# Optimization experiments

Measured on AMD Instinct MI355X. Metric: run time of the kernel, lower is better.

The kernel has to match this reference:

```python
import jax, jax.numpy as jnp
import numpy as np

B, S, D, H, HD = 2, 2048, 1024, 16, 64
K, L = 1024, 4  # num_codes, vq_levels


def setup_inputs() -> dict:
    key = jax.random.key(0)
    ks = jax.random.split(key, 12)
    w = lambda k, shape: jax.random.normal(k, shape, jnp.float32) * 0.02
    return {
        "x": jax.random.normal(ks[0], (B, S, D), jnp.float32),
        "ln1_g": jnp.ones((D,), jnp.float32), "ln1_b": jnp.zeros((D,), jnp.float32),
        "wq": w(ks[1], (D, D)), "wk": w(ks[2], (D, D)), "wv": w(ks[3], (D, D)),
        "wg": w(ks[4], (D, D)), "wo": w(ks[5], (D, D)),
        "ln2_g": jnp.ones((D,), jnp.float32), "ln2_b": jnp.zeros((D,), jnp.float32),
        "w1": w(ks[6], (D, 4 * D)), "b1": jnp.zeros((4 * D,), jnp.float32),
        "w2": w(ks[7], (4 * D, D)), "b2": jnp.zeros((D,), jnp.float32),
        "ln3_g": jnp.ones((D,), jnp.float32), "ln3_b": jnp.zeros((D,), jnp.float32),
        "codebooks": jax.random.uniform(ks[8], (L, K, D), jnp.float32, -1.0 / K, 1.0 / K),
    }


def _ln(x, g, b):
    m = jnp.mean(x, -1, keepdims=True)
    v = jnp.var(x, -1, keepdims=True)
    return (x - m) / jnp.sqrt(v + 1e-5) * g + b


def _rope(x):  # x: [B, S, H, HD]
    hd = x.shape[-1]
    inv = 1.0 / (10000.0 ** (jnp.arange(0, hd, 2, dtype=jnp.float32) / hd))
    t = jnp.arange(x.shape[1], dtype=jnp.float32)
    f = jnp.einsum('i,j->ij', t, inv)               # [S, HD/2]
    emb = jnp.concatenate([f, f], -1)               # [S, HD]
    cos = jnp.cos(emb)[None, :, None, :]
    sin = jnp.sin(emb)[None, :, None, :]
    x1, x2 = jnp.split(x, 2, -1)
    rot = jnp.concatenate([-x2, x1], -1)
    return x * cos + rot * sin


def reference(x, ln1_g, ln1_b, wq, wk, wv, wg, wo, ln2_g, ln2_b,
              w1, b1, w2, b2, ln3_g, ln3_b, codebooks):
    # --- retention sub-block (pre-LN) ---
    h = _ln(x, ln1_g, ln1_b)
    q = (h @ wq).reshape(B, S, H, HD)
    k = (h @ wk).reshape(B, S, H, HD)
    v = (h @ wv).reshape(B, S, H, HD)
    q, k = _rope(q), _rope(k)
    q, k, v = (a.transpose(0, 2, 1, 3) for a in (q, k, v))  # [B,H,S,HD]
    i = jnp.arange(S)
    dmask = jnp.tril(i[:, None] - i[None, :]).astype(jnp.float32)  # [S,S], >=0
    gamma = (1.0 - jnp.exp2(-5.0 - jnp.arange(H, dtype=jnp.float32)))[:, None, None]
    decay = (gamma ** dmask) * jnp.tril(jnp.ones((S, S), jnp.float32))  # [H,S,S]
    ret = jnp.einsum('bhqd,bhkd->bhqk', q, k) / np.sqrt(HD).astype(np.float32) * decay
    o = jnp.einsum('bhqk,bhkd->bhqd', ret, v).transpose(0, 2, 1, 3).reshape(B, S, D)
    g = jax.nn.silu(h @ wg)
    x = x + (o * g) @ wo
    # --- MLP sub-block (pre-LN) ---
    h2 = _ln(x, ln2_g, ln2_b)
    x = x + (jax.nn.gelu(h2 @ w1 + b1, approximate=False) @ w2 + b2)
    # --- residual vector quantizer ---
    xn = _ln(x, ln3_g, ln3_b)
    residual, total = xn, jnp.zeros_like(xn)
    ql, el = 0.0, 0.0
    for lvl in range(L):
        cb = codebooks[lvl]                         # [K, D]
        flat = residual.reshape(-1, D)              # [B*S, D]
        d2 = (jnp.sum(flat ** 2, 1, keepdims=True)
              + jnp.sum(cb ** 2, 1) - 2.0 * flat @ cb.T)
        idx = jnp.argmin(d2, 1)
        quant = cb[idx].reshape(xn.shape)
        ql = ql + jnp.mean((quant - jax.lax.stop_gradient(residual)) ** 2)
        el = el + jnp.mean((jax.lax.stop_gradient(quant) - residual) ** 2)
        total = total + quant
        residual = residual - jax.lax.stop_gradient(quant)
    final = xn + jax.lax.stop_gradient(total - xn)  # straight-through
    return (x + final, ql / L, el / L)
```

## Files before the change

### kernel.cpp

```cpp
#include <hip/hip_runtime.h>
#include <cstdint>
#include <cstddef>

#define DEV __device__ __forceinline__

typedef __attribute__((ext_vector_type(8))) short bf16x8;
typedef __attribute__((ext_vector_type(4))) float f32x4;

typedef const __attribute__((address_space(1))) void gl_void;
typedef __attribute__((address_space(3))) void lds_void;

DEV unsigned short f2bf(float f){
  union { float f; uint32_t u; } v; v.f = f;
  uint32_t r = v.u + 0x7FFFu + ((v.u >> 16) & 1u);
  return (unsigned short)(r >> 16);
}
DEV float bf2f(unsigned short u){
  union { uint32_t u; float f; } v; v.u = ((uint32_t)u) << 16; return v.f;
}
DEV uint32_t packbf2(float a, float b){
  return (uint32_t)f2bf(a) | ((uint32_t)f2bf(b) << 16);
}

__global__ void ln_kernel(const float* __restrict__ x, const float* __restrict__ gw,
                          const float* __restrict__ bw, unsigned short* __restrict__ obf,
                          float* __restrict__ of32)
{
  const int row = blockIdx.x, t = threadIdx.x;
  const float4 v = ((const float4*)(x + (size_t)row*1024))[t];
  float s  = v.x + v.y + v.z + v.w;
  float s2 = v.x*v.x + v.y*v.y + v.z*v.z + v.w*v.w;
  #pragma unroll
  for (int o = 32; o >= 1; o >>= 1){ s += __shfl_down(s, o); s2 += __shfl_down(s2, o); }
  __shared__ float red[8];
  const int w = t >> 6, ln = t & 63;
  if (ln == 0){ red[w] = s; red[4+w] = s2; }
  __syncthreads();
  const float fs  = red[0]+red[1]+red[2]+red[3];
  const float fs2 = red[4]+red[5]+red[6]+red[7];
  const float mean = fs * (1.0f/1024.0f);
  const float var  = fs2 * (1.0f/1024.0f) - mean*mean;
  const float rstd = rsqrtf(var + 1e-5f);
  const float4 gv = ((const float4*)gw)[t];
  const float4 bv = ((const float4*)bw)[t];
  float4 o4;
  o4.x = (v.x-mean)*rstd*gv.x + bv.x;
  o4.y = (v.y-mean)*rstd*gv.y + bv.y;
  o4.z = (v.z-mean)*rstd*gv.z + bv.z;
  o4.w = (v.w-mean)*rstd*gv.w + bv.w;
  if (of32) ((float4*)(of32 + (size_t)row*1024))[t] = o4;
  ushort4 ob; ob.x = f2bf(o4.x); ob.y = f2bf(o4.y); ob.z = f2bf(o4.z); ob.w = f2bf(o4.w);
  ((ushort4*)(obf + (size_t)row*1024))[t] = ob;
}

__global__ void reduce_ln(const float* __restrict__ p, const float* __restrict__ b2,
                          const float* __restrict__ x1, float* __restrict__ x2,
                          const float* __restrict__ g3, const float* __restrict__ b3,
                          unsigned short* __restrict__ resb, float* __restrict__ xnf)
{
  const int row = blockIdx.x, t = threadIdx.x;
  const size_t off = (size_t)row*1024/4 + t;
  const float4 a = ((const float4*)p)[off];
  const float4 b = ((const float4*)(p + 4194304))[off];
  const float4 rv = ((const float4*)x1)[off];
  const float4 bv2 = ((const float4*)b2)[t];
  float4 v;
  v.x = a.x + b.x + rv.x + bv2.x;
  v.y = a.y + b.y + rv.y + bv2.y;
  v.z = a.z + b.z + rv.z + bv2.z;
  v.w = a.w + b.w + rv.w + bv2.w;
  ((float4*)x2)[off] = v;
  float s  = v.x + v.y + v.z + v.w;
  float s2 = v.x*v.x + v.y*v.y + v.z*v.z + v.w*v.w;
  #pragma unroll
  for (int o = 32; o >= 1; o >>= 1){ s += __shfl_down(s, o); s2 += __shfl_down(s2, o); }
  __shared__ float red[8];
  const int w = t >> 6, ln = t & 63;
  if (ln == 0){ red[w] = s; red[4+w] = s2; }
  __syncthreads();
  const float fs  = red[0]+red[1]+red[2]+red[3];
  const float fs2 = red[4]+red[5]+red[6]+red[7];
  const float mean = fs * (1.0f/1024.0f);
  const float var  = fs2 * (1.0f/1024.0f) - mean*mean;
  const float rstd = rsqrtf(var + 1e-5f);
  const float4 gv = ((const float4*)g3)[t];
  const float4 bv = ((const float4*)b3)[t];
  float4 o4;
  o4.x = (v.x-mean)*rstd*gv.x + bv.x;
  o4.y = (v.y-mean)*rstd*gv.y + bv.y;
  o4.z = (v.z-mean)*rstd*gv.z + bv.z;
  o4.w = (v.w-mean)*rstd*gv.w + bv.w;
  ((float4*)xnf)[off] = o4;
  ushort4 ob; ob.x = f2bf(o4.x); ob.y = f2bf(o4.y); ob.z = f2bf(o4.z); ob.w = f2bf(o4.w);
  ((ushort4*)resb)[off] = ob;
}

struct Ptr5 { const float* p[5]; };

DEV void dev_transpose(const float* __restrict__ src, unsigned short* __restrict__ dst,
                       int r0, int c0, int R, int C)
{
  __shared__ float tile[32][33];
  const int tx = threadIdx.x & 31, ty = threadIdx.x >> 5;
  #pragma unroll
  for (int i = 0; i < 32; i += 8)
    tile[ty+i][tx] = src[(size_t)(r0+ty+i)*C + c0 + tx];
  __syncthreads();
  #pragma unroll
  for (int i = 0; i < 32; i += 8)
    dst[(size_t)(c0+ty+i)*R + r0 + tx] = f2bf(tile[tx][ty+i]);
}

__global__ void prep_all(Ptr5 p5, unsigned short* __restrict__ wqkvgT,
                         const float* __restrict__ w1, unsigned short* __restrict__ w1T,
                         const float* __restrict__ w2, unsigned short* __restrict__ w2T,
                         const float* __restrict__ cb, unsigned short* __restrict__ cbbf,
                         float* __restrict__ cbn2, float2* __restrict__ rtab,
                         const float* __restrict__ x, const float* __restrict__ ln1_g,
                         const float* __restrict__ ln1_b, unsigned short* __restrict__ hbf)
{
  const int b = blockIdx.x, t = threadIdx.x;
  if (b < 5120){
    const int z = b >> 10, r = b & 1023;
    dev_transpose(p5.p[z], wqkvgT + (size_t)z*1048576, (r >> 5)*32, (r & 31)*32, 1024, 1024);
  } else if (b < 9216){
    const int r = b - 5120;
    dev_transpose(w1, w1T, (r >> 7)*32, (r & 127)*32, 1024, 4096);
  } else if (b < 13312){
    const int r = b - 9216;
    dev_transpose(w2, w2T, (r >> 5)*32, (r & 31)*32, 4096, 1024);
  } else if (b < 17408){
    const int code = b - 13312;
    const float4 v = ((const float4*)(cb + (size_t)code*1024))[t];
    ushort4 o; o.x = f2bf(v.x); o.y = f2bf(v.y); o.z = f2bf(v.z); o.w = f2bf(v.w);
    ((ushort4*)(cbbf + (size_t)code*1024))[t] = o;
    float s = v.x*v.x + v.y*v.y + v.z*v.z + v.w*v.w;
    #pragma unroll
    for (int off = 32; off >= 1; off >>= 1) s += __shfl_down(s, off);
    __shared__ float red[4];
    if ((t & 63) == 0) red[t >> 6] = s;
    __syncthreads();
    if (t == 0) cbn2[code] = red[0]+red[1]+red[2]+red[3];
  } else if (b < 17664){
    const int i = (b - 17408)*256 + t;
    const int s = i >> 5, j = i & 31;
    const float ang = (float)s * exp2f(-(float)j * 0.4152410118609203f);
    float sn, cs; sincosf(ang, &sn, &cs);
    rtab[i] = make_float2(cs, sn);
  } else {
    const int row = b - 17664;
    const float4 v = ((const float4*)(x + (size_t)row*1024))[t];
    float s  = v.x + v.y + v.z + v.w;
    float s2 = v.x*v.x + v.y*v.y + v.z*v.z + v.w*v.w;
    #pragma unroll
    for (int o = 32; o >= 1; o >>= 1){ s += __shfl_down(s, o); s2 += __shfl_down(s2, o); }
    __shared__ float red2[8];
    const int w = t >> 6, ln = t & 63;
    if (ln == 0){ red2[w] = s; red2[4+w] = s2; }
    __syncthreads();
    const float fs  = red2[0]+red2[1]+red2[2]+red2[3];
    const float fs2 = red2[4]+red2[5]+red2[6]+red2[7];
    const float mean = fs * (1.0f/1024.0f);
    const float var  = fs2 * (1.0f/1024.0f) - mean*mean;
    const float rstd = rsqrtf(var + 1e-5f);
    const float4 gv = ((const float4*)ln1_g)[t];
    const float4 bv = ((const float4*)ln1_b)[t];
    ushort4 ob;
    ob.x = f2bf((v.x-mean)*rstd*gv.x + bv.x);
    ob.y = f2bf((v.y-mean)*rstd*gv.y + bv.y);
    ob.z = f2bf((v.z-mean)*rstd*gv.z + bv.z);
    ob.w = f2bf((v.w-mean)*rstd*gv.w + bv.w);
    ((ushort4*)(hbf + (size_t)row*1024))[t] = ob;
  }
}

template<int EPI>
__global__ __launch_bounds__(512, 2) void gemm256(
    const unsigned short* __restrict__ A, const unsigned short* __restrict__ BT,
    unsigned short* __restrict__ C, const float* __restrict__ bias,
    const float2* __restrict__ rt, int M, int N, int K)
{
  __shared__ __align__(16) unsigned short SH[65536];
  const int t = threadIdx.x;
  const int w = t >> 6, ln = t & 63, lg = ln >> 4, lc = ln & 15;
  const int wm = w >> 2, wn = w & 3;
  const int gx = gridDim.x, nwg = gridDim.x * gridDim.y;
  int lin = blockIdx.y * gx + blockIdx.x;
  lin = (lin >> 3) + (lin & 7) * (nwg >> 3);
  const int m0 = (lin / gx) * 256, n0 = (lin % gx) * 256;
  const int NT = K >> 6;
  const int nit = NT >> 1;

  f32x4 acc[2][2][4][2] = {};
  bf16x8 aF[4][2], bF[2][2];

  auto stageHT = [&](int d, int isB, int h, int kt){
    const unsigned short* src = isB ? BT : A;
    const int mb = (isB ? n0 : m0) + h*128;
    const int base16 = isB*4096 + d*2048 + h*1024;
    #pragma unroll
    for (int j = 0; j < 2; ++j){
      const int o = j*512 + t;
      const int wu = o & 63;
      const int r16 = wu >> 2, cu = wu & 3;
      const int s = o >> 6;
      const int rg = s >> 1, cg = s & 1;
      const int row = rg*16 + r16;
      const int srcu = cg*4 + (cu ^ ((r16 & 8) >> 2));
      __builtin_amdgcn_global_load_lds(
        (gl_void*)(src + (size_t)(mb + row)*K + (size_t)kt*64 + srcu*8),
        (lds_void*)&SH[(base16 + j*512 + (t & ~63))*8], 16, 0, 0);
    }
  };

  auto ldA = [&](int d, int mh, int mf, int ks) -> bf16x8 {
    const int u = d*2048 + mh*1024 + ((wm*4+mf)*2 + ks)*64 + lc*4 + (lg ^ ((lc & 8) >> 2));
    return *(const bf16x8*)&SH[u*8];
  };
  auto ldB = [&](int d, int nh, int nf, int ks) -> bf16x8 {
    const int u = 4096 + d*2048 + nh*1024 + ((wn*2+nf)*2 + ks)*64 + lc*4 + (lg ^ ((lc & 8) >> 2));
    return *(const bf16x8*)&SH[u*8];
  };

#define RD_A(d, mh) { _Pragma("unroll") for (int mf = 0; mf < 4; ++mf){ \
    aF[mf][0] = ldA(d, mh, mf, 0); aF[mf][1] = ldA(d, mh, mf, 1); } }
#define RD_B(d, nh) { _Pragma("unroll") for (int nf = 0; nf < 2; ++nf){ \
    bF[nf][0] = ldB(d, nh, nf, 0); bF[nf][1] = ldB(d, nh, nf, 1); } }
#define MM(mh, nh) { \
    __builtin_amdgcn_s_setprio(1); \
    _Pragma("unroll") for (int mf = 0; mf < 4; ++mf) \
      _Pragma("unroll") for (int nf = 0; nf < 2; ++nf){ \
        acc[mh][nh][mf][nf] = __builtin_amdgcn_mfma_f32_16x16x32_bf16(aF[mf][0], bF[nf][0], acc[mh][nh][mf][nf], 0, 0, 0); \
        acc[mh][nh][mf][nf] = __builtin_amdgcn_mfma_f32_16x16x32_bf16(aF[mf][1], bF[nf][1], acc[mh][nh][mf][nf], 0, 0, 0); } \
    __builtin_amdgcn_s_setprio(0); }
#define BAR()   __builtin_amdgcn_s_barrier()
#define LGKM0() asm volatile("s_waitcnt lgkmcnt(0)" ::: "memory")

  stageHT(0,0,0,0); stageHT(0,0,1,0); stageHT(0,1,0,0); stageHT(0,1,1,0);
  stageHT(1,0,0,1); stageHT(1,1,1,1);
  asm volatile("s_waitcnt vmcnt(4)" ::: "memory");
  BAR();

  for (int it = 0; it < nit; ++it){
    const int v = 2*it + 1, up = 2*it + 2, vp = 2*it + 3;
    const bool hu = (up < NT), hv = (vp < NT);

    RD_A(0,0); RD_B(0,0);
    stageHT(1,0,1,v);
    BAR(); LGKM0(); MM(0,0); BAR();

    RD_B(0,1);
    stageHT(1,1,0,v);
    BAR(); LGKM0(); MM(0,1); BAR();

    RD_A(0,1);
    if (hu) stageHT(0,0,0,up);
    BAR(); LGKM0(); MM(1,1); BAR();

    RD_B(0,0);
    if (hu) stageHT(0,1,1,up);
    BAR(); LGKM0(); MM(1,0);
    if (hu) asm volatile("s_waitcnt vmcnt(4)" ::: "memory");
    else    asm volatile("s_waitcnt vmcnt(0)" ::: "memory");
    BAR();

    RD_A(1,0); RD_B(1,0);
    if (hu) stageHT(0,0,1,up);
    BAR(); LGKM0(); MM(0,0); BAR();

    RD_B(1,1);
    if (hu) stageHT(0,1,0,up);
    BAR(); LGKM0(); MM(0,1); BAR();

    RD_A(1,1);
    if (hv) stageHT(1,0,0,vp);
    BAR(); LGKM0(); MM(1,1); BAR();

    RD_B(1,0);
    if (hv) stageHT(1,1,1,vp);
    BAR(); LGKM0(); MM(1,0);
    if (hv) asm volatile("s_waitcnt vmcnt(4)" ::: "memory");
    else    asm volatile("s_waitcnt vmcnt(0)" ::: "memory");
    BAR();
  }
#undef RD_A
#undef RD_B
#undef MM

  const int sect = n0 >> 10;
  unsigned short* outp3 = C + (size_t)sect*4194304;
  const int cb1 = n0 & 1023;
  unsigned short* slab = &SH[wm*4096];

  #pragma unroll
  for (int mh = 0; mh < 2; ++mh){
    #pragma unroll
    for (int mf = 0; mf < 4; ++mf){
      BAR();
      #pragma unroll
      for (int nh = 0; nh < 2; ++nh)
        #pragma unroll
        for (int nf = 0; nf < 2; ++nf)
          #pragma unroll
          for (int r = 0; r < 4; ++r){
            const int rho = lg*4 + r;
            const int c = nh*128 + wn*32 + nf*16 + lc;
            float vv = acc[mh][nh][mf][nf][r];
            if constexpr (EPI == 2){
              vv += bias[n0 + c];
              vv = 0.5f * vv * (1.0f + erff(vv * 0.70710678118654752f));
            }
            if constexpr (EPI == 3){ if (sect == 3) vv = vv * (1.0f / (1.0f + __expf(-vv))); }
            slab[rho*256 + ((((c>>3) ^ (rho&3)))<<3) + (c&7)] = f2bf(vv);
          }
      LGKM0();
      BAR();
      const int rr = ln >> 2;
      const int row = m0 + mh*128 + wm*64 + mf*16 + rr;
      #pragma unroll
      for (int kk = 0; kk < 2; ++kk){
        const int cc = wn*64 + (ln & 3)*16 + kk*8;
        const int u = cc >> 3;
        const bf16x8 vown = *(const bf16x8*)&slab[rr*256 + ((u ^ (rr&3))<<3)];
        if constexpr (EPI == 3){
          if (sect <= 1){
            const bf16x8 vpart = *(const bf16x8*)&slab[rr*256 + (((u^4) ^ (rr&3))<<3)];
            const int s_ = row & 2047;
            union { bf16x8 v; unsigned short s[8]; } ov, pv, res;
            ov.v = vown; pv.v = vpart;
            #pragma unroll
            for (int j = 0; j < 8; ++j){
              const int col = cc + j;
              const float2 cs = rt[(s_ << 5) + (col & 31)];
              const float a = bf2f(ov.s[j]), b = bf2f(pv.s[j]);
              res.s[j] = f2bf((col & 32) ? (a*cs.x + b*cs.y) : (a*cs.x - b*cs.y));
            }
            *(bf16x8*)(outp3 + (size_t)row*1024 + cb1 + cc) = res.v;
          } else {
            *(bf16x8*)(outp3 + (size_t)row*1024 + cb1 + cc) = vown;
          }
        } else {
          *(bf16x8*)(C + (size_t)row*N + n0 + cc) = vown;
        }
      }
    }
  }
#undef BAR
#undef LGKM0
}

template<int NSPLIT>
__global__ __launch_bounds__(256, 4) void gemm128_sk(
    const unsigned short* __restrict__ A, const unsigned short* __restrict__ BT,
    float* __restrict__ Cp_base, int M, int N, int K)
{
  __shared__ __align__(16) unsigned short As[2][128*32];
  __shared__ __align__(16) unsigned short Bs[2][128*32];
  const int t = threadIdx.x;
  const int w = t >> 6, ln = t & 63, lg = ln >> 4, lc = ln & 15;
  const int gx = gridDim.x, nwg = gridDim.x * gridDim.y;
  int lin = blockIdx.y * gx + blockIdx.x;
  lin = (lin >> 3) + (lin & 7) * (nwg >> 3);
  const int m0 = (lin / gx) * 128, n0 = (lin % gx) * 128;
  const int wr = (w >> 1) * 64, wc = (w & 1) * 64;
  f32x4 acc[4][4] = {};
  const int nkt = (K >> 5) / NSPLIT;
  const int ktb = blockIdx.z * nkt;

  auto stage = [&](int buf, int kt){
    #pragma unroll
    for (int c = 0; c < 2; ++c){
      const int chunk = c*256 + t;
      const int row = chunk >> 2, ke = (chunk & 3) * 8;
      __builtin_amdgcn_global_load_lds(
          (gl_void*)(A + (size_t)(m0+row)*K + (size_t)(ktb+kt)*32 + ke),
          (lds_void*)&As[buf][(c*256 + w*64)*8], 16, 0, 0);
      __builtin_amdgcn_global_load_lds(
          (gl_void*)(BT + (size_t)(n0+row)*K + (size_t)(ktb+kt)*32 + ke),
          (lds_void*)&Bs[buf][(c*256 + w*64)*8], 16, 0, 0);
    }
  };

  stage(0, 0);
  __syncthreads();
  for (int kt = 0; kt < nkt; ++kt){
    const int cur = kt & 1;
    if (kt + 1 < nkt) stage(cur ^ 1, kt + 1);
    bf16x8 af[4], bfr[4];
    #pragma unroll
    for (int i = 0; i < 4; ++i){
      af[i]  = *(const bf16x8*)&As[cur][(wr + i*16 + lc)*32 + lg*8];
      bfr[i] = *(const bf16x8*)&Bs[cur][(wc + i*16 + lc)*32 + lg*8];
    }
    #pragma unroll
    for (int m = 0; m < 4; ++m)
      #pragma unroll
      for (int n = 0; n < 4; ++n)
        acc[m][n] = __builtin_amdgcn_mfma_f32_16x16x32_bf16(af[m], bfr[n], acc[m][n], 0, 0, 0);
    __syncthreads();
  }

  float* Cp = Cp_base + (size_t)blockIdx.z * (size_t)M * N;
  #pragma unroll
  for (int m = 0; m < 4; ++m)
    #pragma unroll
    for (int n = 0; n < 4; ++n)
      #pragma unroll
      for (int r = 0; r < 4; ++r){
        const int row = m0 + wr + m*16 + lg*4 + r;
        const int col = n0 + wc + n*16 + lc;
        Cp[(size_t)row*N + col] = acc[m][n][r];
      }
}

template<int EPI, bool BIAS, bool RES, bool OUTBF>
__global__ __launch_bounds__(256, 3) void gemm64_bt(
    const unsigned short* __restrict__ A, const unsigned short* __restrict__ BT,
    void* __restrict__ Cv, const float* __restrict__ bias, const float* __restrict__ resid,
    int M, int N, int K)
{
  __shared__ __align__(16) unsigned short As[2][64*64];
  __shared__ __align__(16) unsigned short Bs[2][128*64];
  const int t = threadIdx.x;
  const int w = t >> 6, ln = t & 63, lg = ln >> 4, lc = ln & 15;
  const int gx = gridDim.x, nwg = gridDim.x * gridDim.y;
  int lin = blockIdx.y * gx + blockIdx.x;
  lin = (lin >> 3) + (lin & 7) * (nwg >> 3);
  const int bx = lin % gx, by = lin / gx;
  const int m0 = by * 64, n0 = bx * 128;
  const int wr = (w >> 1) * 32, wc = (w & 1) * 64;
  f32x4 acc[2][4] = {};
  const int nkt = K >> 6;

  auto stage = [&](int buf, int kt){
    #pragma unroll
    for (int c = 0; c < 2; ++c){
      const int chunk = c*256 + t;
      const int row = chunk >> 3;
      const int kb = (((chunk & 7) << 4) ^ ((row & 7) << 4)) >> 1;
      __builtin_amdgcn_global_load_lds(
          (gl_void*)(A + (size_t)(m0+row)*K + (size_t)kt*64 + kb),
          (lds_void*)&As[buf][(c*256 + w*64)*8], 16, 0, 0);
    }
    #pragma unroll
    for (int c = 0; c < 4; ++c){
      const int chunk = c*256 + t;
      const int row = chunk >> 3;
      const int kb = (((chunk & 7) << 4) ^ ((row & 7) << 4)) >> 1;
      __builtin_amdgcn_global_load_lds(
          (gl_void*)(BT + (size_t)(n0+row)*K + (size_t)kt*64 + kb),
          (lds_void*)&Bs[buf][(c*256 + w*64)*8], 16, 0, 0);
    }
  };

  stage(0, 0);
  __syncthreads();
  for (int kt = 0; kt < nkt; ++kt){
    const int cur = kt & 1;
    if (kt + 1 < nkt) stage(cur ^ 1, kt + 1);
    #pragma unroll
    for (int ks = 0; ks < 2; ++ks){
      bf16x8 af[2], bfr[4];
      #pragma unroll
      for (int i = 0; i < 2; ++i){
        const int rowA = wr + i*16 + lc;
        const int colA = (((ks<<6) + (lg<<4)) ^ ((rowA & 7) << 4)) >> 1;
        af[i] = *(const bf16x8*)&As[cur][rowA*64 + colA];
      }
      #pragma unroll
      for (int i = 0; i < 4; ++i){
        const int rowB = wc + i*16 + lc;
        const int colB = (((ks<<6) + (lg<<4)) ^ ((rowB & 7) << 4)) >> 1;
        bfr[i] = *(const bf16x8*)&Bs[cur][rowB*64 + colB];
      }
      #pragma unroll
      for (int m = 0; m < 2; ++m)
        #pragma unroll
        for (int n = 0; n < 4; ++n)
          acc[m][n] = __builtin_amdgcn_mfma_f32_16x16x32_bf16(af[m], bfr[n], acc[m][n], 0, 0, 0);
    }
    __syncthreads();
  }

  if constexpr (EPI == 4){
    #pragma unroll
    for (int m = 0; m < 2; ++m){
      #pragma unroll
      for (int r = 0; r < 4; ++r){
        float best = 3.4e38f; int bi = 0;
        #pragma unroll
        for (int n = 0; n < 4; ++n){
          const int col = n0 + wc + n*16 + lc;
          const float d = bias[col] - 2.0f*acc[m][n][r];
          if (d < best){ best = d; bi = col; }
        }
        #pragma unroll
        for (int o = 1; o < 16; o <<= 1){
          const float ob = __shfl_xor(best, o);
          const int oi = __shfl_xor(bi, o);
          if (ob < best || (ob == best && oi < bi)){ best = ob; bi = oi; }
        }
        if (lc == 0){
          const int row = m0 + wr + m*16 + lg*4 + r;
          ((float2*)Cv)[row*16 + bx*2 + (w & 1)] = make_float2(best, (float)bi);
        }
      }
    }
    return;
  }

  #pragma unroll
  for (int m = 0; m < 2; ++m){
    #pragma unroll
    for (int n = 0; n < 4; ++n){
      #pragma unroll
      for (int r = 0; r < 4; ++r){
        const int row = m0 + wr + m*16 + lg*4 + r;
        const int col = n0 + wc + n*16 + lc;
        float v = acc[m][n][r];
        if constexpr (BIAS) v += bias[col];
        if constexpr (RES) v += resid[(size_t)row*N + col];
        if constexpr (OUTBF) ((unsigned short*)Cv)[(size_t)row*N + col] = f2bf(v);
        else                 ((float*)Cv)[(size_t)row*N + col] = v;
      }
    }
  }
}

__global__ __launch_bounds__(256, 2) void chunk_sum(
    const unsigned short* __restrict__ kb, const unsigned short* __restrict__ vb,
    unsigned short* __restrict__ Tbuf)
{
  __shared__ unsigned short KT[64*72];
  __shared__ unsigned short VT[64*72];
  const int t = threadIdx.x, w = t >> 6, ln = t & 63, lg = ln >> 4, lc = ln & 15;
  const int blk = blockIdx.x;
  const int bh = blk >> 5, c = blk & 31;
  const int b = bh >> 4, hh = bh & 15;
  const float lg2g = log2f(1.0f - exp2f(-5.0f - (float)hh));
  #pragma unroll
  for (int ch = 0; ch < 2; ++ch){
    const int chunk = ch*256 + t;
    const int i = chunk >> 3, d0 = (chunk & 7)*8;
    const size_t gofs = ((size_t)(b*2048 + c*64 + i))*1024 + hh*64 + d0;
    const float wi = exp2f(lg2g * (float)(64 - i));
    union {uint4 u; unsigned short s[8];} kv, vv;
    kv.u = *(const uint4*)(kb + gofs);
    vv.u = *(const uint4*)(vb + gofs);
    #pragma unroll
    for (int j = 0; j < 8; ++j){
      KT[(d0+j)*72 + i] = f2bf(bf2f(kv.s[j]) * wi);
      VT[(d0+j)*72 + i] = vv.s[j];
    }
  }
  __syncthreads();
  f32x4 acc[4] = {};
  #pragma unroll
  for (int ks = 0; ks < 2; ++ks){
    const bf16x8 af = *(const bf16x8*)&KT[(w*16 + lc)*72 + ks*32 + lg*8];
    #pragma unroll
    for (int n = 0; n < 4; ++n){
      const bf16x8 bf = *(const bf16x8*)&VT[(n*16 + lc)*72 + ks*32 + lg*8];
      acc[n] = __builtin_amdgcn_mfma_f32_16x16x32_bf16(af, bf, acc[n], 0, 0, 0);
    }
  }
  unsigned short* out = Tbuf + (size_t)blk*4096;
  #pragma unroll
  for (int n = 0; n < 4; ++n)
    #pragma unroll
    for (int r = 0; r < 4; ++r)
      out[(w*16 + lg*4 + r)*64 + n*16 + lc] = f2bf(acc[n][r]);
}

__global__ void chunk_scan(const unsigned short* __restrict__ Tbuf, unsigned short* __restrict__ statesT)
{
  const int bh = blockIdx.x, q = blockIdx.y, t = threadIdx.x;
  const int hh = bh & 15;
  const float gamma = 1.0f - exp2f(-5.0f - (float)hh);
  const float g64 = exp2f(log2f(gamma) * 64.0f);
  float S[4] = {0.f, 0.f, 0.f, 0.f};
  const int dv = t >> 2;
  const int j0 = q*16 + (t & 3)*4;
  for (int c = 0; c < 32; ++c){
    const size_t base = ((size_t)(bh*32 + c))*4096;
    ushort4 p; p.x = f2bf(S[0]); p.y = f2bf(S[1]); p.z = f2bf(S[2]); p.w = f2bf(S[3]);
    *(ushort4*)(statesT + base + dv*64 + j0) = p;
    #pragma unroll
    for (int j = 0; j < 4; ++j)
      S[j] = g64*S[j] + bf2f(Tbuf[base + (size_t)(j0 + j)*64 + dv]);
  }
}

__global__ __launch_bounds__(256, 2) void retention_chunk(
    const unsigned short* __restrict__ qb, const unsigned short* __restrict__ kb,
    const unsigned short* __restrict__ vb, const unsigned short* __restrict__ gb,
    const unsigned short* __restrict__ statesT, unsigned short* __restrict__ og)
{
  __shared__ unsigned short VT[64*72];
  __shared__ unsigned short Pw[64*72];
  const int t = threadIdx.x, w = t >> 6, ln = t & 63, lg = ln >> 4, lc = ln & 15;
  const int blk = blockIdx.x;
  const int bh = blk >> 5, c = blk & 31;
  const int b = bh >> 4, hh = bh & 15;
  const float lg2g = log2f(1.0f - exp2f(-5.0f - (float)hh));
  float gpr[4];
  #pragma unroll
  for (int r = 0; r < 4; ++r) gpr[r] = exp2f(-lg2g * (float)r);
  const size_t rowbase = (size_t)(b*2048 + c*64);

  #pragma unroll
  for (int ch = 0; ch < 2; ++ch){
    const int chunk = ch*256 + t;
    const int i = chunk >> 3, d0 = (chunk & 7)*8;
    union {uint4 u; unsigned short s[8];} vv;
    vv.u = *(const uint4*)(vb + (rowbase + i)*1024 + hh*64 + d0);
    #pragma unroll
    for (int j = 0; j < 8; ++j) VT[(d0+j)*72 + i] = vv.s[j];
  }

  bf16x8 Qf[2], Kf[4][2];
  #pragma unroll
  for (int ks = 0; ks < 2; ++ks){
    union {uint4 u; bf16x8 f;} cv;
    cv.u = *(const uint4*)(qb + (rowbase + w*16 + lc)*1024 + hh*64 + ks*32 + lg*8);
    Qf[ks] = cv.f;
    #pragma unroll
    for (int mt = 0; mt < 4; ++mt){
      union {uint4 u; bf16x8 f;} kv;
      kv.u = *(const uint4*)(kb + (rowbase + mt*16 + lc)*1024 + hh*64 + ks*32 + lg*8);
      Kf[mt][ks] = kv.f;
    }
  }

  f32x4 st[4] = {};
  #pragma unroll
  for (int ks = 0; ks < 2; ++ks)
    #pragma unroll
    for (int mt = 0; mt < 4; ++mt)
      st[mt] = __builtin_amdgcn_mfma_f32_16x16x32_bf16(Kf[mt][ks], Qf[ks], st[mt], 0, 0, 0);

  __syncthreads();

  #pragma unroll
  for (int mt = 0; mt < 4; ++mt){
    const int kp = mt*16 + lg*4;
    const int qrow = w*16 + lc;
    const int delta0 = qrow - kp;
    const float dec0 = exp2f(lg2g * (float)delta0) * 0.125f;
    float vals[4];
    #pragma unroll
    for (int r = 0; r < 4; ++r)
      vals[r] = (delta0 >= r) ? st[mt][r] * dec0 * gpr[r] : 0.0f;
    uint2 pk; pk.x = packbf2(vals[0], vals[1]); pk.y = packbf2(vals[2], vals[3]);
    *(uint2*)&Pw[qrow*72 + kp] = pk;
  }

  f32x4 acc[4] = {};
  const unsigned short* Sbase = statesT + (size_t)blk*4096;
  #pragma unroll
  for (int ks = 0; ks < 2; ++ks)
    #pragma unroll
    for (int n = 0; n < 4; ++n){
      union {uint4 u; bf16x8 f;} sv;
      sv.u = *(const uint4*)(Sbase + (n*16 + lc)*64 + ks*32 + lg*8);
      acc[n] = __builtin_amdgcn_mfma_f32_16x16x32_bf16(Qf[ks], sv.f, acc[n], 0, 0, 0);
    }
  #pragma unroll
  for (int n = 0; n < 4; ++n)
    #pragma unroll
    for (int r = 0; r < 4; ++r)
      acc[n][r] *= exp2f(lg2g * (float)(w*16 + lg*4 + r)) * 0.125f;

  #pragma unroll
  for (int ks = 0; ks < 2; ++ks){
    const bf16x8 Pf = *(const bf16x8*)&Pw[(w*16 + lc)*72 + ks*32 + lg*8];
    #pragma unroll
    for (int n = 0; n < 4; ++n){
      const bf16x8 Vf = *(const bf16x8*)&VT[(n*16 + lc)*72 + ks*32 + lg*8];
      acc[n] = __builtin_amdgcn_mfma_f32_16x16x32_bf16(Pf, Vf, acc[n], 0, 0, 0);
    }
  }

  #pragma unroll
  for (int n = 0; n < 4; ++n){
    #pragma unroll
    for (int r = 0; r < 4; ++r){
      const size_t row = rowbase + w*16 + lg*4 + r;
      const int col = hh*64 + n*16 + lc;
      const float gv = bf2f(gb[row*1024 + col]);
      og[row*1024 + col] = f2bf(acc[n][r] * gv);
    }
  }
}

template<int FINAL>
__global__ void rvq_update4(const unsigned short* __restrict__ cbbf_l,
                            const float2* __restrict__ partials,
                            unsigned short* __restrict__ resb, float* __restrict__ qlpart, int lvl,
                            const float* __restrict__ x2, const float* __restrict__ xn,
                            float* __restrict__ outf)
{
  const int m = blockIdx.x, t = threadIdx.x;
  __shared__ int sid;
  if (t == 0){
    float best = 3.4e38f; int bi = 0;
    #pragma unroll
    for (int p = 0; p < 16; ++p){
      const float2 pr = partials[m*16 + p];
      if (pr.x < best){ best = pr.x; bi = (int)pr.y; }
    }
    sid = bi;
  }
  __syncthreads();
  const int id = sid;
  const ushort4 qv = ((const ushort4*)(cbbf_l + (size_t)id*1024))[t];
  const ushort4 rv = ((const ushort4*)(resb + (size_t)m*1024))[t];
  const float n0 = bf2f(rv.x) - bf2f(qv.x);
  const float n1 = bf2f(rv.y) - bf2f(qv.y);
  const float n2 = bf2f(rv.z) - bf2f(qv.z);
  const float n3 = bf2f(rv.w) - bf2f(qv.w);
  if constexpr (FINAL){
    const size_t off = (size_t)m*256 + t;
    const float4 a = ((const float4*)x2)[off];
    const float4 b = ((const float4*)xn)[off];
    float4 o;
    o.x = a.x + b.x - n0;
    o.y = a.y + b.y - n1;
    o.z = a.z + b.z - n2;
    o.w = a.w + b.w - n3;
    ((float4*)outf)[off] = o;
  } else {
    ushort4 nb; nb.x = f2bf(n0); nb.y = f2bf(n1); nb.z = f2bf(n2); nb.w = f2bf(n3);
    ((ushort4*)(resb + (size_t)m*1024))[t] = nb;
  }
  float s = n0*n0 + n1*n1 + n2*n2 + n3*n3;
  #pragma unroll
  for (int o = 32; o >= 1; o >>= 1) s += __shfl_down(s, o);
  __shared__ float red[4];
  if ((t & 63) == 0) red[t >> 6] = s;
  __syncthreads();
  if (t == 0) qlpart[lvl*4096 + m] = red[0]+red[1]+red[2]+red[3];
}

__global__ void ql_final(const float* __restrict__ qlpart, float* __restrict__ outs)
{
  const int t = threadIdx.x;
  float s = 0.f;
  for (int i = t; i < 16384; i += 1024) s += qlpart[i];
  #pragma unroll
  for (int o = 32; o >= 1; o >>= 1) s += __shfl_down(s, o);
  __shared__ float red[16];
  if ((t & 63) == 0) red[t >> 6] = s;
  __syncthreads();
  if (t == 0){
    float q = 0.f;
    #pragma unroll
    for (int i = 0; i < 16; ++i) q += red[i];
    q *= (1.0f/4194304.0f) * 0.25f;
    outs[0] = q; outs[1] = q;
  }
}

extern "C" void kernel_launch(void* const* d_in, const int* in_sizes, int n_in,
                              void* d_out, int out_size, void* d_ws, size_t ws_size,
                              hipStream_t stream)
{
  const float* x     = (const float*)d_in[0];
  const float* ln1_g = (const float*)d_in[1];
  const float* ln1_b = (const float*)d_in[2];
  const float* wq    = (const float*)d_in[3];
  const float* wk    = (const float*)d_in[4];
  const float* wv    = (const float*)d_in[5];
  const float* wg    = (const float*)d_in[6];
  const float* wo    = (const float*)d_in[7];
  const float* ln2_g = (const float*)d_in[8];
  const float* ln2_b = (const float*)d_in[9];
  const float* w1    = (const float*)d_in[10];
  const float* b1    = (const float*)d_in[11];
  const float* w2    = (const float*)d_in[12];
  const float* b2    = (const float*)d_in[13];
  const float* ln3_g = (const float*)d_in[14];
  const float* ln3_b = (const float*)d_in[15];
  const float* cb    = (const float*)d_in[16];

  char* ws = (char*)d_ws;
  const size_t MB = 1024*1024;
  unsigned short* wqkvgT = (unsigned short*)(ws + 0*MB);
  unsigned short* w1T  = (unsigned short*)(ws + 10*MB);
  unsigned short* w2T  = (unsigned short*)(ws + 18*MB);
  unsigned short* cbbf = (unsigned short*)(ws + 26*MB);
  float* cbn2     = (float*)(ws + 34*MB);
  float* qlpart   = (float*)(ws + 34*MB + 16*1024);
  float2* partials= (float2*)(ws + 34*MB + 128*1024);
  unsigned short* hbf  = (unsigned short*)(ws + 35*MB);
  unsigned short* qbuf = (unsigned short*)(ws + 43*MB);
  unsigned short* kbuf = (unsigned short*)(ws + 51*MB);
  unsigned short* vbuf = (unsigned short*)(ws + 59*MB);
  unsigned short* gbuf = (unsigned short*)(ws + 67*MB);
  float* skbuf  = (float*)(ws + 43*MB);
  unsigned short* ogb  = (unsigned short*)(ws + 75*MB);
  float* x1     = (float*)(ws + 83*MB);
  unsigned short* h2   = (unsigned short*)(ws + 99*MB);
  unsigned short* a1   = (unsigned short*)(ws + 107*MB);
  float* x2     = (float*)(ws + 139*MB);
  unsigned short* Tbuf = (unsigned short*)(ws + 139*MB);
  float* xnf    = (float*)(ws + 155*MB);
  unsigned short* statesT = (unsigned short*)(ws + 155*MB);
  unsigned short* resb = (unsigned short*)(ws + 171*MB);
  float2* rtab  = (float2*)(ws + 179*MB);

  float* outf = (float*)d_out;

  Ptr5 p5; p5.p[0]=wq; p5.p[1]=wk; p5.p[2]=wv; p5.p[3]=wg; p5.p[4]=wo;
  hipLaunchKernelGGL(prep_all, dim3(21760), dim3(256), 0, stream,
                     p5, wqkvgT, w1, w1T, w2, w2T, cb, cbbf, cbn2, rtab,
                     x, ln1_g, ln1_b, hbf);

  hipLaunchKernelGGL((gemm256<3>), dim3(16,16), dim3(512), 0, stream,
                     hbf, wqkvgT, qbuf, (const float*)nullptr, (const float2*)rtab, 4096, 4096, 1024);
  hipLaunchKernelGGL(chunk_sum,  dim3(1024), dim3(256), 0, stream, kbuf, vbuf, Tbuf);
  hipLaunchKernelGGL(chunk_scan, dim3(32,4), dim3(256), 0, stream, Tbuf, statesT);
  hipLaunchKernelGGL(retention_chunk, dim3(1024), dim3(256), 0, stream,
                     qbuf, kbuf, vbuf, gbuf, statesT, ogb);
  hipLaunchKernelGGL((gemm64_bt<0,false,true,false>), dim3(8,64), dim3(256), 0, stream,
                     ogb, wqkvgT + 4194304, (void*)x1, (const float*)nullptr, x, 4096, 1024, 1024);

  hipLaunchKernelGGL(ln_kernel, dim3(4096), dim3(256), 0, stream, x1, ln2_g, ln2_b, h2, (float*)nullptr);
  hipLaunchKernelGGL((gemm256<2>), dim3(16,16), dim3(512), 0, stream,
                     h2, w1T, a1, b1, (const float2*)rtab, 4096, 4096, 1024);
  hipLaunchKernelGGL((gemm128_sk<2>), dim3(8,32,2), dim3(256), 0, stream,
                     a1, w2T, skbuf, 4096, 1024, 4096);
  hipLaunchKernelGGL(reduce_ln, dim3(4096), dim3(256), 0, stream,
                     skbuf, b2, x1, x2, ln3_g, ln3_b, resb, xnf);

  for (int lvl = 0; lvl < 4; ++lvl){
    hipLaunchKernelGGL((gemm64_bt<4,false,false,false>), dim3(8,64), dim3(256), 0, stream,
                       resb, cbbf + (size_t)lvl*1048576, (void*)partials,
                       cbn2 + lvl*1024, (const float*)nullptr, 4096, 1024, 1024);
    if (lvl < 3)
      hipLaunchKernelGGL((rvq_update4<0>), dim3(4096), dim3(256), 0, stream,
                         cbbf + (size_t)lvl*1048576, partials, resb, qlpart, lvl,
                         (const float*)nullptr, (const float*)nullptr, (float*)nullptr);
    else
      hipLaunchKernelGGL((rvq_update4<1>), dim3(4096), dim3(256), 0, stream,
                         cbbf + (size_t)lvl*1048576, partials, resb, qlpart, lvl,
                         x2, xnf, outf);
  }

  hipLaunchKernelGGL(ql_final, dim3(1), dim3(1024), 0, stream, qlpart, outf + 4194304);
}
```

Before: 372.6 us.

## Replace 256x256 GEMM with 128x256 triple-buffered kernel and direct-store epilogue

The two 4096x4096x1024 GEMMs (QKVG projection with RoPE/SiLU epilogue, and W1 with GELU) move from a 256x256 tile with a hand-scheduled 64-wide K pipeline to a 128x256 tile with 32-wide K steps and a three-stage LDS ring buffer. LDS use drops and the grid doubles to 512 workgroups, which may improve occupancy and load balance. The epilogue stops staging through LDS and writes bf16 scalars straight from the accumulators, computing RoPE in fp32 from the paired accumulator. The cost is less operand reuse per tile, more barriers per K step, and uncoalesced 2-byte global stores.

```diff
diff --git a/kernel.cpp b/kernel.cpp
--- a/kernel.cpp
+++ b/kernel.cpp
@@ -175,178 +175,134 @@
 }
 
 template<int EPI>
-__global__ __launch_bounds__(512, 2) void gemm256(
+__global__ __launch_bounds__(512, 2) void gemmf(
     const unsigned short* __restrict__ A, const unsigned short* __restrict__ BT,
     unsigned short* __restrict__ C, const float* __restrict__ bias,
     const float2* __restrict__ rt, int M, int N, int K)
 {
-  __shared__ __align__(16) unsigned short SH[65536];
+  __shared__ __align__(16) unsigned short SH[36864];
   const int t = threadIdx.x;
   const int w = t >> 6, ln = t & 63, lg = ln >> 4, lc = ln & 15;
   const int wm = w >> 2, wn = w & 3;
   const int gx = gridDim.x, nwg = gridDim.x * gridDim.y;
   int lin = blockIdx.y * gx + blockIdx.x;
   lin = (lin >> 3) + (lin & 7) * (nwg >> 3);
-  const int m0 = (lin / gx) * 256, n0 = (lin % gx) * 256;
-  const int NT = K >> 6;
-  const int nit = NT >> 1;
-
-  f32x4 acc[2][2][4][2] = {};
-  bf16x8 aF[4][2], bF[2][2];
-
-  auto stageHT = [&](int d, int isB, int h, int kt){
-    const unsigned short* src = isB ? BT : A;
-    const int mb = (isB ? n0 : m0) + h*128;
-    const int base16 = isB*4096 + d*2048 + h*1024;
+  const int m0 = (lin / gx) * 128, n0 = (lin % gx) * 256;
+  const int nkt = K >> 5;
+
+  f32x4 acc[4][4] = {};
+  bf16x8 aF[4], bF[4];
+
+  auto stage = [&](int buf, int kt){
+    const int ub = buf*1536;
+    {
+      const int ro = t >> 2, cu = t & 3;
+      const int su = cu ^ ((ro >> 1) & 3);
+      __builtin_amdgcn_global_load_lds(
+        (gl_void*)(A + (size_t)(m0+ro)*K + (size_t)kt*32 + su*8),
+        (lds_void*)&SH[(ub + (t & ~63))*8], 16, 0, 0);
+    }
     #pragma unroll
     for (int j = 0; j < 2; ++j){
-      const int o = j*512 + t;
-      const int wu = o & 63;
-      const int r16 = wu >> 2, cu = wu & 3;
-      const int s = o >> 6;
-      const int rg = s >> 1, cg = s & 1;
-      const int row = rg*16 + r16;
-      const int srcu = cg*4 + (cu ^ ((r16 & 8) >> 2));
+      const int u = j*512 + t;
+      const int ro = u >> 2, cu = u & 3;
+      const int su = cu ^ ((ro >> 1) & 3);
       __builtin_amdgcn_global_load_lds(
-        (gl_void*)(src + (size_t)(mb + row)*K + (size_t)kt*64 + srcu*8),
-        (lds_void*)&SH[(base16 + j*512 + (t & ~63))*8], 16, 0, 0);
+        (gl_void*)(BT + (size_t)(n0+ro)*K + (size_t)kt*32 + su*8),
+        (lds_void*)&SH[(ub + 512 + j*512 + (t & ~63))*8], 16, 0, 0);
     }
   };
 
-  auto ldA = [&](int d, int mh, int mf, int ks) -> bf16x8 {
-    const int u = d*2048 + mh*1024 + ((wm*4+mf)*2 + ks)*64 + lc*4 + (lg ^ ((lc & 8) >> 2));
-    return *(const bf16x8*)&SH[u*8];
+  auto ldA = [&](int buf, int mf) -> bf16x8 {
+    const int R = wm*64 + mf*16 + lc;
+    const int cu = lg ^ ((R >> 1) & 3);
+    return *(const bf16x8*)&SH[(buf*1536 + R*4 + cu)*8];
   };
-  auto ldB = [&](int d, int nh, int nf, int ks) -> bf16x8 {
-    const int u = 4096 + d*2048 + nh*1024 + ((wn*2+nf)*2 + ks)*64 + lc*4 + (lg ^ ((lc & 8) >> 2));
-    return *(const bf16x8*)&SH[u*8];
+  auto ldB = [&](int buf, int nf) -> bf16x8 {
+    const int R = wn*64 + nf*16 + lc;
+    const int cu = lg ^ ((R >> 1) & 3);
+    return *(const bf16x8*)&SH[(buf*1536 + 512 + R*4 + cu)*8];
   };
 
-#define RD_A(d, mh) { _Pragma("unroll") for (int mf = 0; mf < 4; ++mf){ \
-    aF[mf][0] = ldA(d, mh, mf, 0); aF[mf][1] = ldA(d, mh, mf, 1); } }
-#define RD_B(d, nh) { _Pragma("unroll") for (int nf = 0; nf < 2; ++nf){ \
-    bF[nf][0] = ldB(d, nh, nf, 0); bF[nf][1] = ldB(d, nh, nf, 1); } }
-#define MM(mh, nh) { \
-    __builtin_amdgcn_s_setprio(1); \
-    _Pragma("unroll") for (int mf = 0; mf < 4; ++mf) \
-      _Pragma("unroll") for (int nf = 0; nf < 2; ++nf){ \
-        acc[mh][nh][mf][nf] = __builtin_amdgcn_mfma_f32_16x16x32_bf16(aF[mf][0], bF[nf][0], acc[mh][nh][mf][nf], 0, 0, 0); \
-        acc[mh][nh][mf][nf] = __builtin_amdgcn_mfma_f32_16x16x32_bf16(aF[mf][1], bF[nf][1], acc[mh][nh][mf][nf], 0, 0, 0); } \
-    __builtin_amdgcn_s_setprio(0); }
-#define BAR()   __builtin_amdgcn_s_barrier()
-#define LGKM0() asm volatile("s_waitcnt lgkmcnt(0)" ::: "memory")
-
-  stageHT(0,0,0,0); stageHT(0,0,1,0); stageHT(0,1,0,0); stageHT(0,1,1,0);
-  stageHT(1,0,0,1); stageHT(1,1,1,1);
-  asm volatile("s_waitcnt vmcnt(4)" ::: "memory");
-  BAR();
-
-  for (int it = 0; it < nit; ++it){
-    const int v = 2*it + 1, up = 2*it + 2, vp = 2*it + 3;
-    const bool hu = (up < NT), hv = (vp < NT);
-
-    RD_A(0,0); RD_B(0,0);
-    stageHT(1,0,1,v);
-    BAR(); LGKM0(); MM(0,0); BAR();
-
-    RD_B(0,1);
-    stageHT(1,1,0,v);
-    BAR(); LGKM0(); MM(0,1); BAR();
-
-    RD_A(0,1);
-    if (hu) stageHT(0,0,0,up);
-    BAR(); LGKM0(); MM(1,1); BAR();
-
-    RD_B(0,0);
-    if (hu) stageHT(0,1,1,up);
-    BAR(); LGKM0(); MM(1,0);
-    if (hu) asm volatile("s_waitcnt vmcnt(4)" ::: "memory");
+  stage(0, 0); stage(1, 1);
+  asm volatile("s_waitcnt vmcnt(3)" ::: "memory");
+  __builtin_amdgcn_s_barrier();
+
+  for (int kt = 0; kt < nkt; ++kt){
+    const int cur = kt % 3;
+    const bool pf = (kt + 2 < nkt);
+
+    if (pf) stage((kt + 2) % 3, kt + 2);
+    #pragma unroll
+    for (int f = 0; f < 4; ++f) aF[f] = ldA(cur, f);
+    bF[0] = ldB(cur, 0); bF[1] = ldB(cur, 1);
+    __builtin_amdgcn_s_barrier();
+    __builtin_amdgcn_s_setprio(1);
+    #pragma unroll
+    for (int mf = 0; mf < 4; ++mf)
+      #pragma unroll
+      for (int nf = 0; nf < 2; ++nf)
+        acc[mf][nf] = __builtin_amdgcn_mfma_f32_16x16x32_bf16(aF[mf], bF[nf], acc[mf][nf], 0, 0, 0);
+    __builtin_amdgcn_s_setprio(0);
+    asm volatile("s_waitcnt lgkmcnt(0)" ::: "memory");
+    __builtin_amdgcn_s_barrier();
+
+    bF[2] = ldB(cur, 2); bF[3] = ldB(cur, 3);
+    __builtin_amdgcn_s_barrier();
+    __builtin_amdgcn_s_setprio(1);
+    #pragma unroll
+    for (int mf = 0; mf < 4; ++mf)
+      #pragma unroll
+      for (int nf = 2; nf < 4; ++nf)
+        acc[mf][nf] = __builtin_amdgcn_mfma_f32_16x16x32_bf16(aF[mf], bF[nf], acc[mf][nf], 0, 0, 0);
+    __builtin_amdgcn_s_setprio(0);
+    asm volatile("s_waitcnt lgkmcnt(0)" ::: "memory");
+    if (pf) asm volatile("s_waitcnt vmcnt(3)" ::: "memory");
     else    asm volatile("s_waitcnt vmcnt(0)" ::: "memory");
-    BAR();
-
-    RD_A(1,0); RD_B(1,0);
-    if (hu) stageHT(0,0,1,up);
-    BAR(); LGKM0(); MM(0,0); BAR();
-
-    RD_B(1,1);
-    if (hu) stageHT(0,1,0,up);
-    BAR(); LGKM0(); MM(0,1); BAR();
-
-    RD_A(1,1);
-    if (hv) stageHT(1,0,0,vp);
-    BAR(); LGKM0(); MM(1,1); BAR();
-
-    RD_B(1,0);
-    if (hv) stageHT(1,1,1,vp);
-    BAR(); LGKM0(); MM(1,0);
-    if (hv) asm volatile("s_waitcnt vmcnt(4)" ::: "memory");
-    else    asm volatile("s_waitcnt vmcnt(0)" ::: "memory");
-    BAR();
-  }
-#undef RD_A
-#undef RD_B
-#undef MM
-
-  const int sect = n0 >> 10;
-  unsigned short* outp3 = C + (size_t)sect*4194304;
-  const int cb1 = n0 & 1023;
-  unsigned short* slab = &SH[wm*4096];
-
-  #pragma unroll
-  for (int mh = 0; mh < 2; ++mh){
+    __builtin_amdgcn_s_barrier();
+  }
+
+  if constexpr (EPI == 3){
+    const int sect = n0 >> 10;
+    unsigned short* outp = C + (size_t)sect*4194304;
+    const int cb1 = n0 & 1023;
     #pragma unroll
     for (int mf = 0; mf < 4; ++mf){
-      BAR();
-      #pragma unroll
-      for (int nh = 0; nh < 2; ++nh)
+      #pragma unroll
+      for (int r = 0; r < 4; ++r){
+        const int row = m0 + wm*64 + mf*16 + lg*4 + r;
+        const int s_ = row & 2047;
         #pragma unroll
-        for (int nf = 0; nf < 2; ++nf)
-          #pragma unroll
-          for (int r = 0; r < 4; ++r){
-            const int rho = lg*4 + r;
-            const int c = nh*128 + wn*32 + nf*16 + lc;
-            float vv = acc[mh][nh][mf][nf][r];
-            if constexpr (EPI == 2){
-              vv += bias[n0 + c];
-              vv = 0.5f * vv * (1.0f + erff(vv * 0.70710678118654752f));
-            }
-            if constexpr (EPI == 3){ if (sect == 3) vv = vv * (1.0f / (1.0f + __expf(-vv))); }
-            slab[rho*256 + ((((c>>3) ^ (rho&3)))<<3) + (c&7)] = f2bf(vv);
+        for (int nf = 0; nf < 4; ++nf){
+          const int c1 = cb1 + wn*64 + nf*16 + lc;
+          float v = acc[mf][nf][r];
+          if (sect <= 1){
+            const float2 cs = rt[(s_ << 5) + (c1 & 31)];
+            const float vp = acc[mf][nf ^ 2][r];
+            v = (c1 & 32) ? (v*cs.x + vp*cs.y) : (v*cs.x - vp*cs.y);
+          } else if (sect == 3){
+            v = v * (1.0f / (1.0f + __expf(-v)));
           }
-      LGKM0();
-      BAR();
-      const int rr = ln >> 2;
-      const int row = m0 + mh*128 + wm*64 + mf*16 + rr;
-      #pragma unroll
-      for (int kk = 0; kk < 2; ++kk){
-        const int cc = wn*64 + (ln & 3)*16 + kk*8;
-        const int u = cc >> 3;
-        const bf16x8 vown = *(const bf16x8*)&slab[rr*256 + ((u ^ (rr&3))<<3)];
-        if constexpr (EPI == 3){
-          if (sect <= 1){
-            const bf16x8 vpart = *(const bf16x8*)&slab[rr*256 + (((u^4) ^ (rr&3))<<3)];
-            const int s_ = row & 2047;
-            union { bf16x8 v; unsigned short s[8]; } ov, pv, res;
-            ov.v = vown; pv.v = vpart;
-            #pragma unroll
-            for (int j = 0; j < 8; ++j){
-              const int col = cc + j;
-              const float2 cs = rt[(s_ << 5) + (col & 31)];
-              const float a = bf2f(ov.s[j]), b = bf2f(pv.s[j]);
-              res.s[j] = f2bf((col & 32) ? (a*cs.x + b*cs.y) : (a*cs.x - b*cs.y));
-            }
-            *(bf16x8*)(outp3 + (size_t)row*1024 + cb1 + cc) = res.v;
-          } else {
-            *(bf16x8*)(outp3 + (size_t)row*1024 + cb1 + cc) = vown;
-          }
-        } else {
-          *(bf16x8*)(C + (size_t)row*N + n0 + cc) = vown;
+          outp[(size_t)row*1024 + c1] = f2bf(v);
         }
       }
     }
-  }
-#undef BAR
-#undef LGKM0
+  } else {
+    #pragma unroll
+    for (int mf = 0; mf < 4; ++mf){
+      #pragma unroll
+      for (int r = 0; r < 4; ++r){
+        const int row = m0 + wm*64 + mf*16 + lg*4 + r;
+        #pragma unroll
+        for (int nf = 0; nf < 4; ++nf){
+          const int col = n0 + wn*64 + nf*16 + lc;
+          float v = acc[mf][nf][r] + bias[col];
+          v = 0.5f * v * (1.0f + erff(v * 0.70710678118654752f));
+          C[(size_t)row*N + col] = f2bf(v);
+        }
+      }
+    }
+  }
 }
 
 template<int NSPLIT>
@@ -816,7 +772,7 @@
                      p5, wqkvgT, w1, w1T, w2, w2T, cb, cbbf, cbn2, rtab,
                      x, ln1_g, ln1_b, hbf);
 
-  hipLaunchKernelGGL((gemm256<3>), dim3(16,16), dim3(512), 0, stream,
+  hipLaunchKernelGGL((gemmf<3>), dim3(16,32), dim3(512), 0, stream,
                      hbf, wqkvgT, qbuf, (const float*)nullptr, (const float2*)rtab, 4096, 4096, 1024);
   hipLaunchKernelGGL(chunk_sum,  dim3(1024), dim3(256), 0, stream, kbuf, vbuf, Tbuf);
   hipLaunchKernelGGL(chunk_scan, dim3(32,4), dim3(256), 0, stream, Tbuf, statesT);
@@ -826,7 +782,7 @@
                      ogb, wqkvgT + 4194304, (void*)x1, (const float*)nullptr, x, 4096, 1024, 1024);
 
   hipLaunchKernelGGL(ln_kernel, dim3(4096), dim3(256), 0, stream, x1, ln2_g, ln2_b, h2, (float*)nullptr);
-  hipLaunchKernelGGL((gemm256<2>), dim3(16,16), dim3(512), 0, stream,
+  hipLaunchKernelGGL((gemmf<2>), dim3(16,32), dim3(512), 0, stream,
                      h2, w1T, a1, b1, (const float2*)rtab, 4096, 4096, 1024);
   hipLaunchKernelGGL((gemm128_sk<2>), dim3(8,32,2), dim3(256), 0, stream,
                      a1, w2T, skbuf, 4096, 1024, 4096);
```

Result: no change. 373.7 us (+0.3%).
